# Optimization experiments

Measured on AMD Instinct MI355X. Metric: run time of the kernel, lower is better.

The kernel has to match this reference:

```python
import jax, jax.numpy as jnp
from jax import lax
import numpy as np

UNITS = 256
DYN = 32
STATIC = 27


def setup_inputs() -> dict:
    key = jax.random.key(0)
    ks = jax.random.split(key, 7)
    x_dynamic = jax.random.normal(ks[0], (1024, 365, DYN), dtype=jnp.float32)
    x_static = jax.random.normal(ks[1], (1024, STATIC), dtype=jnp.float32)
    # learned parameters (orthogonal-ish init approximated by scaled normals;
    # weight_hh initialized as tiled identity per the original module)
    weight_ih = jax.random.normal(ks[2], (DYN, 3 * UNITS), dtype=jnp.float32) * 0.1
    eye3 = jnp.concatenate([jnp.eye(UNITS, dtype=jnp.float32)] * 3, axis=1)
    weight_hh = eye3 + jax.random.normal(ks[3], (UNITS, 3 * UNITS), dtype=jnp.float32) * 0.02
    weight_sh = jax.random.normal(ks[4], (STATIC, UNITS), dtype=jnp.float32) * 0.1
    bias = jnp.zeros((3 * UNITS,), dtype=jnp.float32)
    bias_s = jnp.zeros((UNITS,), dtype=jnp.float32)
    return {
        "x_dynamic": x_dynamic,
        "x_static": x_static,
        "weight_ih": weight_ih,
        "weight_hh": weight_hh,
        "weight_sh": weight_sh,
        "bias": bias,
        "bias_s": bias_s,
    }


def reference(x_dynamic, x_static, weight_ih, weight_hh, weight_sh, bias, bias_s):
    B = x_dynamic.shape[0]
    U = weight_sh.shape[1]
    # static input gate, computed once (entity-aware)
    i_gate = jax.nn.sigmoid(x_static @ weight_sh + bias_s)  # [B, U]
    # precompute input contribution for all timesteps: [B, T, 3U]
    gx = jnp.einsum("btd,dk->btk", x_dynamic, weight_ih) + bias
    gx_t = jnp.swapaxes(gx, 0, 1)  # [T, B, 3U] for scan

    h0 = jnp.zeros((B, U), dtype=x_dynamic.dtype)
    c0 = jnp.zeros((B, U), dtype=x_dynamic.dtype)

    def step(carry, g_t):
        h, c = carry
        gates = g_t + h @ weight_hh  # [B, 3U]
        f, o, g = jnp.split(gates, 3, axis=1)
        c_new = jax.nn.sigmoid(f) * c + i_gate * jnp.tanh(g)
        h_new = jax.nn.sigmoid(o) * jnp.tanh(c_new)
        return (h_new, c_new), None

    (h_final, c_final), _ = lax.scan(step, (h0, c0), gx_t)
    return h_final
```

## Files before the change

kernel.cpp:

```cpp
#include <hip/hip_runtime.h>


typedef short short8 __attribute__((ext_vector_type(8)));
typedef short short4s __attribute__((ext_vector_type(4)));
typedef float f32x4 __attribute__((ext_vector_type(4)));
typedef int   i32x4 __attribute__((ext_vector_type(4)));

#define T_STEPS 365
#define UNITS   256
#define G3      768
#define MROWS   4
#define NWGS    256
#define HP8     288
#define XROW    (T_STEPS * 32)
#define XPAD    96
#define WP8_BYTES (256 * G3)

__device__ __forceinline__ unsigned short f2bf(float x) {
    union { float f; unsigned u; } v; v.f = x;
    return (unsigned short)((v.u + 0x7FFFu + ((v.u >> 16) & 1u)) >> 16);
}
__device__ __forceinline__ float rcp_(float x) {
    float r; asm("v_rcp_f32 %0, %1" : "=v"(r) : "v"(x)); return r;
}
__device__ __forceinline__ float sigm_(float x) {
    return rcp_(1.0f + __expf(-x));
}
__device__ __forceinline__ float tanh_(float x) {
    return 1.0f - 2.0f * rcp_(1.0f + __expf(2.0f * x));
}
__device__ __forceinline__ f32x4 MF(short8 a, short8 b, f32x4 c) {
    return __builtin_amdgcn_mfma_f32_16x16x32_bf16(a, b, c, 0, 0, 0);
}
__device__ __forceinline__ i32x4 MI(i32x4 a, i32x4 b, i32x4 c) {
    return __builtin_amdgcn_mfma_i32_16x16x64_i8(a, b, c, 0, 0, 0);
}

__global__ __launch_bounds__(256) void pack_weights(
    const float* __restrict__ w_ih, const float* __restrict__ w_hh,
    signed char* __restrict__ wp8, unsigned short* __restrict__ wpx)
{
    int idx = blockIdx.x * 256 + threadIdx.x;
    if (idx < 256 * G3) {
        const int k = idx / G3, n = idx - k * G3;
        float v = w_hh[k * G3 + n];
        if ((n & 255) == k) v -= 1.0f;
        int q = (int)rintf(v * 1024.0f);
        q = q > 127 ? 127 : (q < -127 ? -127 : q);
        wp8[((size_t)((k >> 6) * G3) + n) * 64 + (k & 63)] = (signed char)q;
    } else if (idx < (256 + 32) * G3) {
        const int idx2 = idx - 256 * G3;
        const int kx = idx2 / G3, n = idx2 - kx * G3;
        wpx[((size_t)((kx >> 3) * G3) + n) * 8 + (kx & 7)] = f2bf(w_ih[kx * G3 + n]);
    }
}

#define STEP_BODY(E, FC, FN, DOX, LOADX, W) do {                              \
    const int p_ = (E) & 1;                                                   \
    __syncthreads();                                                          \
    const signed char* Ap_ = &A_s[p_][0][0];                                  \
    const i32x4 a0_ = *(const i32x4*)(Ap_ + abase);                           \
    const i32x4 a1_ = *(const i32x4*)(Ap_ + abase + 64);                      \
    const i32x4 a2_ = *(const i32x4*)(Ap_ + abase + 128);                     \
    const i32x4 a3_ = *(const i32x4*)(Ap_ + abase + 192);                     \
        \
    i32x4 if0_ = MI(a0_, bwi[0][0][0], IZERO);                                \
    i32x4 io0_ = MI(a0_, bwi[0][1][0], IZERO);                                \
    i32x4 ig0_ = MI(a0_, bwi[0][2][0], IZERO);                                \
    if0_ = MI(a1_, bwi[1][0][0], if0_);                                       \
    io0_ = MI(a1_, bwi[1][1][0], io0_);                                       \
    ig0_ = MI(a1_, bwi[1][2][0], ig0_);                                       \
    if0_ = MI(a2_, bwi[2][0][0], if0_);                                       \
    io0_ = MI(a2_, bwi[2][1][0], io0_);                                       \
    ig0_ = MI(a2_, bwi[2][2][0], ig0_);                                       \
    if0_ = MI(a3_, bwi[3][0][0], if0_);                                       \
    io0_ = MI(a3_, bwi[3][1][0], io0_);                                       \
    ig0_ = MI(a3_, bwi[3][2][0], ig0_);                                       \
    i32x4 if1_ = MI(a0_, bwi[0][0][1], IZERO);                                \
    i32x4 io1_ = MI(a0_, bwi[0][1][1], IZERO);                                \
    i32x4 ig1_ = MI(a0_, bwi[0][2][1], IZERO);                                \
    if1_ = MI(a1_, bwi[1][0][1], if1_);                                       \
    io1_ = MI(a1_, bwi[1][1][1], io1_);                                       \
    ig1_ = MI(a1_, bwi[1][2][1], ig1_);                                       \
    if1_ = MI(a2_, bwi[2][0][1], if1_);                                       \
    io1_ = MI(a2_, bwi[2][1][1], io1_);                                       \
    ig1_ = MI(a2_, bwi[2][2][1], ig1_);                                       \
    if1_ = MI(a3_, bwi[3][0][1], if1_);                                       \
    io1_ = MI(a3_, bwi[3][1][1], io1_);                                       \
    ig1_ = MI(a3_, bwi[3][2][1], ig1_);                                       \
    if (DOX) {                                                                \
           \
        const short8 xu_ = xa;                                                \
        FN[0] = MF(xu_, bwx[0][0], FZERO);                                    \
        FN[1] = MF(xu_, bwx[1][0], FZERO);                                    \
        FN[2] = MF(xu_, bwx[2][0], FZERO);                                    \
        FN[3] = MF(xu_, bwx[0][1], FZERO);                                    \
        FN[4] = MF(xu_, bwx[1][1], FZERO);                                    \
        FN[5] = MF(xu_, bwx[2][1], FZERO);                                    \
        if (LOADX)                                                            \
            xa = *(const short8*)(xq + (size_t)((W) + 2) * 128);              \
    }                                                                         \
    {         \
        const float bh_ = hp[0];                                              \
        const float gf_ = FC[0][E] + bfv[0] + bh_ + (float)if0_[0] * SCL;     \
        const float go_ = FC[1][E] + bov[0] + bh_ + (float)io0_[0] * SCL;     \
        const float gg_ = FC[2][E] + bgv[0] + bh_ + (float)ig0_[0] * SCL;     \
        const float f_  = sigm_(gf_);                                         \
        const float o_  = sigm_(go_);                                         \
        const float gt_ = tanh_(gg_);                                         \
        const float cn_ = f_ * cc[0] + ig[0] * gt_;                           \
        cc[0] = cn_;                                                          \
        const float hn_ = o_ * tanh_(cn_);                                    \
        hp[0] = hn_;                                                          \
        A_s[p_ ^ 1][qq][u0] = (signed char)__float2int_rn(hn_ * 127.0f);      \
    }                                                                         \
    {                                                           \
        const float bh_ = hp[1];                                              \
        const float gf_ = FC[3][E] + bfv[1] + bh_ + (float)if1_[0] * SCL;     \
        const float go_ = FC[4][E] + bov[1] + bh_ + (float)io1_[0] * SCL;     \
        const float gg_ = FC[5][E] + bgv[1] + bh_ + (float)ig1_[0] * SCL;     \
        const float f_  = sigm_(gf_);                                         \
        const float o_  = sigm_(go_);                                         \
        const float gt_ = tanh_(gg_);                                         \
        const float cn_ = f_ * cc[1] + ig[1] * gt_;                           \
        cc[1] = cn_;                                                          \
        const float hn_ = o_ * tanh_(cn_);                                    \
        hp[1] = hn_;                                                          \
        A_s[p_ ^ 1][qq][u1] = (signed char)__float2int_rn(hn_ * 127.0f);      \
    }                                                                         \
} while (0)

#define WINDOW4(W, FC, FN, LOADX) do {                                        \
    STEP_BODY(0, FC, FN, false, false, W);                                    \
    STEP_BODY(1, FC, FN, true,  LOADX, W);                                    \
    STEP_BODY(2, FC, FN, false, false, W);                                    \
    STEP_BODY(3, FC, FN, false, false, W);                                    \
} while (0)

__global__ __launch_bounds__(512, 2) void lstm_mfma(
    const float* __restrict__ x_dyn,
    const float* __restrict__ x_sta,
    const signed char* __restrict__ wp8,
    const unsigned short* __restrict__ wpx,
    const float* __restrict__ w_sh,
    const float* __restrict__ bias,
    const float* __restrict__ bias_s,
    float* __restrict__ out)
{
    __shared__ signed char A_s[2][MROWS][HP8];
    __shared__ unsigned short xs[MROWS * XROW + XPAD];

    const int tid  = threadIdx.x;
    const int b0   = blockIdx.x * MROWS;
    const int lane = tid & 63;
    const int wv   = tid >> 6;
    const int mm   = lane & 15;
    const int qq   = lane >> 4;

    i32x4 bwi[4][3][2];
    #pragma unroll
    for (int ks = 0; ks < 4; ++ks)
        #pragma unroll
        for (int g = 0; g < 3; ++g)
            #pragma unroll
            for (int h = 0; h < 2; ++h) {
                const int n = g * UNITS + wv * 32 + h * 16 + mm;
                bwi[ks][g][h] = *(const i32x4*)(wp8 +
                    ((size_t)(ks * G3) + n) * 64 + qq * 16);
            }
    short8 bwx[3][2];
    #pragma unroll
    for (int g = 0; g < 3; ++g)
        #pragma unroll
        for (int h = 0; h < 2; ++h)
            bwx[g][h] = *(const short8*)(wpx +
                ((size_t)(qq * G3) + g * UNITS + wv * 32 + h * 16 + mm) * 8);

    #pragma unroll
    for (int r = 0; r < MROWS; ++r) {
        const float4* src = (const float4*)(x_dyn + (size_t)(b0 + r) * XROW);
        short4s* dst = (short4s*)(xs + r * XROW);
        for (int i = tid; i < XROW / 4; i += 512) {
            const float4 v = src[i];
            short4s w;
            w.x = (short)f2bf(v.x); w.y = (short)f2bf(v.y);
            w.z = (short)f2bf(v.z); w.w = (short)f2bf(v.w);
            dst[i] = w;
        }
    }
    if (tid < XPAD / 2) ((int*)(xs + MROWS * XROW))[tid] = 0;
    {
        int* az = (int*)A_s;
        for (int i = tid; i < 2 * MROWS * HP8 / 4; i += 512) az[i] = 0;
    }
    __syncthreads();

    const int u0 = wv * 32 + mm;
    const int u1 = u0 + 16;

    const float bfv[2] = { bias[u0],             bias[u1] };
    const float bov[2] = { bias[UNITS + u0],     bias[UNITS + u1] };
    const float bgv[2] = { bias[2 * UNITS + u0], bias[2 * UNITS + u1] };

    float ig[2], cc[2], hp[2];
    #pragma unroll
    for (int h = 0; h < 2; ++h) {
        const int u = h ? u1 : u0;
        float s = bias_s[u];
        #pragma unroll
        for (int j = 0; j < 27; ++j)
            s += x_sta[(b0 + qq) * 27 + j] * w_sh[j * UNITS + u];
        ig[h] = sigm_(s);
        cc[h] = 0.0f; hp[h] = 0.0f;
    }

    const int abase = (mm >> 2) * HP8 + qq * 16;
    const unsigned short* xq = xs + (size_t)(mm >> 2) * XROW + (mm & 3) * 32 + qq * 8;
    const float SCL = 1.0f / (127.0f * 1024.0f);
    const f32x4 FZERO = {0.f, 0.f, 0.f, 0.f};
    const i32x4 IZERO = {0, 0, 0, 0};

    f32x4 FA[6], FB[6];
    short8 xa;
    {
        const short8 x0 = *(const short8*)(xq);
        FA[0] = MF(x0, bwx[0][0], FZERO);
        FA[1] = MF(x0, bwx[1][0], FZERO);
        FA[2] = MF(x0, bwx[2][0], FZERO);
        FA[3] = MF(x0, bwx[0][1], FZERO);
        FA[4] = MF(x0, bwx[1][1], FZERO);
        FA[5] = MF(x0, bwx[2][1], FZERO);
        xa = *(const short8*)(xq + 128);
    }

    for (int wp = 0; wp < 45; ++wp) {
        const int w0 = wp * 2;
        WINDOW4(w0,     FA, FB, true);
        WINDOW4(w0 + 1, FB, FA, true);
    }
    WINDOW4(90, FA, FB, false);
    STEP_BODY(0, FB, FA, false, false, 91);

    out[(size_t)(b0 + qq) * UNITS + u0] = hp[0];
    out[(size_t)(b0 + qq) * UNITS + u1] = hp[1];
}

extern "C" void kernel_launch(void* const* d_in, const int* in_sizes, int n_in,
                              void* d_out, int out_size, void* d_ws, size_t ws_size,
                              hipStream_t stream) {
    const float* x_dyn  = (const float*)d_in[0];
    const float* x_sta  = (const float*)d_in[1];
    const float* w_ih   = (const float*)d_in[2];
    const float* w_hh   = (const float*)d_in[3];
    const float* w_sh   = (const float*)d_in[4];
    const float* bias   = (const float*)d_in[5];
    const float* bias_s = (const float*)d_in[6];
    float* out = (float*)d_out;
    signed char* wp8 = (signed char*)d_ws;
    unsigned short* wpx = (unsigned short*)((char*)d_ws + WP8_BYTES);

    pack_weights<<<((256 + 32) * G3 + 255) / 256, 256, 0, stream>>>(w_ih, w_hh, wp8, wpx);
    lstm_mfma<<<NWGS, 512, 0, stream>>>(x_dyn, x_sta, wp8, wpx, w_sh, bias, bias_s, out);
}
```

Baseline: 348.9 us.

## Split MFMA accumulation chains, raise MFMA priority, pack adjacent-unit h stores

Each gate accumulation is split into two independent MFMA chains (k-slices 0-1 and 2-3) that are summed in integer afterwards, shortening the dependent chain on the recurrent critical path. The MFMA block is wrapped in s_setprio to favour this wave's matrix issue. Each lane now owns units 2*mm and 2*mm+1 instead of mm and mm+16, so the two quantized h bytes go out as one 16-bit LDS store and the final output as a float2 store. This costs extra accumulator registers and integer adds, and changes the weight and bias indexing layout.

```diff
diff --git a/kernel.cpp b/kernel.cpp
--- a/kernel.cpp
+++ b/kernel.cpp
@@ -63,33 +63,22 @@
     const i32x4 a1_ = *(const i32x4*)(Ap_ + abase + 64);                      \
     const i32x4 a2_ = *(const i32x4*)(Ap_ + abase + 128);                     \
     const i32x4 a3_ = *(const i32x4*)(Ap_ + abase + 192);                     \
-        \
-    i32x4 if0_ = MI(a0_, bwi[0][0][0], IZERO);                                \
-    i32x4 io0_ = MI(a0_, bwi[0][1][0], IZERO);                                \
-    i32x4 ig0_ = MI(a0_, bwi[0][2][0], IZERO);                                \
-    if0_ = MI(a1_, bwi[1][0][0], if0_);                                       \
-    io0_ = MI(a1_, bwi[1][1][0], io0_);                                       \
-    ig0_ = MI(a1_, bwi[1][2][0], ig0_);                                       \
-    if0_ = MI(a2_, bwi[2][0][0], if0_);                                       \
-    io0_ = MI(a2_, bwi[2][1][0], io0_);                                       \
-    ig0_ = MI(a2_, bwi[2][2][0], ig0_);                                       \
-    if0_ = MI(a3_, bwi[3][0][0], if0_);                                       \
-    io0_ = MI(a3_, bwi[3][1][0], io0_);                                       \
-    ig0_ = MI(a3_, bwi[3][2][0], ig0_);                                       \
-    i32x4 if1_ = MI(a0_, bwi[0][0][1], IZERO);                                \
-    i32x4 io1_ = MI(a0_, bwi[0][1][1], IZERO);                                \
-    i32x4 ig1_ = MI(a0_, bwi[0][2][1], IZERO);                                \
-    if1_ = MI(a1_, bwi[1][0][1], if1_);                                       \
-    io1_ = MI(a1_, bwi[1][1][1], io1_);                                       \
-    ig1_ = MI(a1_, bwi[1][2][1], ig1_);                                       \
-    if1_ = MI(a2_, bwi[2][0][1], if1_);                                       \
-    io1_ = MI(a2_, bwi[2][1][1], io1_);                                       \
-    ig1_ = MI(a2_, bwi[2][2][1], ig1_);                                       \
-    if1_ = MI(a3_, bwi[3][0][1], if1_);                                       \
-    io1_ = MI(a3_, bwi[3][1][1], io1_);                                       \
-    ig1_ = MI(a3_, bwi[3][2][1], ig1_);                                       \
+    __builtin_amdgcn_s_setprio(1);                                            \
+                     \
+    i32x4 ifA0_ = MI(a1_, bwi[1][0][0], MI(a0_, bwi[0][0][0], IZERO));        \
+    i32x4 ioA0_ = MI(a1_, bwi[1][1][0], MI(a0_, bwi[0][1][0], IZERO));        \
+    i32x4 igA0_ = MI(a1_, bwi[1][2][0], MI(a0_, bwi[0][2][0], IZERO));        \
+    i32x4 ifB0_ = MI(a3_, bwi[3][0][0], MI(a2_, bwi[2][0][0], IZERO));        \
+    i32x4 ioB0_ = MI(a3_, bwi[3][1][0], MI(a2_, bwi[2][1][0], IZERO));        \
+    i32x4 igB0_ = MI(a3_, bwi[3][2][0], MI(a2_, bwi[2][2][0], IZERO));        \
+    i32x4 ifA1_ = MI(a1_, bwi[1][0][1], MI(a0_, bwi[0][0][1], IZERO));        \
+    i32x4 ioA1_ = MI(a1_, bwi[1][1][1], MI(a0_, bwi[0][1][1], IZERO));        \
+    i32x4 igA1_ = MI(a1_, bwi[1][2][1], MI(a0_, bwi[0][2][1], IZERO));        \
+    i32x4 ifB1_ = MI(a3_, bwi[3][0][1], MI(a2_, bwi[2][0][1], IZERO));        \
+    i32x4 ioB1_ = MI(a3_, bwi[3][1][1], MI(a2_, bwi[2][1][1], IZERO));        \
+    i32x4 igB1_ = MI(a3_, bwi[3][2][1], MI(a2_, bwi[2][2][1], IZERO));        \
     if (DOX) {                                                                \
-           \
+                              \
         const short8 xu_ = xa;                                                \
         FN[0] = MF(xu_, bwx[0][0], FZERO);                                    \
         FN[1] = MF(xu_, bwx[1][0], FZERO);                                    \
@@ -100,11 +89,16 @@
         if (LOADX)                                                            \
             xa = *(const short8*)(xq + (size_t)((W) + 2) * 128);              \
     }                                                                         \
-    {         \
+    __builtin_amdgcn_s_setprio(0);                                            \
+    int q0_, q1_;                                                             \
+    {                      \
         const float bh_ = hp[0];                                              \
-        const float gf_ = FC[0][E] + bfv[0] + bh_ + (float)if0_[0] * SCL;     \
-        const float go_ = FC[1][E] + bov[0] + bh_ + (float)io0_[0] * SCL;     \
-        const float gg_ = FC[2][E] + bgv[0] + bh_ + (float)ig0_[0] * SCL;     \
+        const float gf_ = FC[0][E] + bfv[0] + bh_                             \
+                        + (float)(ifA0_[0] + ifB0_[0]) * SCL;                 \
+        const float go_ = FC[1][E] + bov[0] + bh_                             \
+                        + (float)(ioA0_[0] + ioB0_[0]) * SCL;                 \
+        const float gg_ = FC[2][E] + bgv[0] + bh_                             \
+                        + (float)(igA0_[0] + igB0_[0]) * SCL;                 \
         const float f_  = sigm_(gf_);                                         \
         const float o_  = sigm_(go_);                                         \
         const float gt_ = tanh_(gg_);                                         \
@@ -112,13 +106,16 @@
         cc[0] = cn_;                                                          \
         const float hn_ = o_ * tanh_(cn_);                                    \
         hp[0] = hn_;                                                          \
-        A_s[p_ ^ 1][qq][u0] = (signed char)__float2int_rn(hn_ * 127.0f);      \
+        q0_ = __float2int_rn(hn_ * 127.0f);                                   \
     }                                                                         \
     {                                                           \
         const float bh_ = hp[1];                                              \
-        const float gf_ = FC[3][E] + bfv[1] + bh_ + (float)if1_[0] * SCL;     \
-        const float go_ = FC[4][E] + bov[1] + bh_ + (float)io1_[0] * SCL;     \
-        const float gg_ = FC[5][E] + bgv[1] + bh_ + (float)ig1_[0] * SCL;     \
+        const float gf_ = FC[3][E] + bfv[1] + bh_                             \
+                        + (float)(ifA1_[0] + ifB1_[0]) * SCL;                 \
+        const float go_ = FC[4][E] + bov[1] + bh_                             \
+                        + (float)(ioA1_[0] + ioB1_[0]) * SCL;                 \
+        const float gg_ = FC[5][E] + bgv[1] + bh_                             \
+                        + (float)(igA1_[0] + igB1_[0]) * SCL;                 \
         const float f_  = sigm_(gf_);                                         \
         const float o_  = sigm_(go_);                                         \
         const float gt_ = tanh_(gg_);                                         \
@@ -126,8 +123,11 @@
         cc[1] = cn_;                                                          \
         const float hn_ = o_ * tanh_(cn_);                                    \
         hp[1] = hn_;                                                          \
-        A_s[p_ ^ 1][qq][u1] = (signed char)__float2int_rn(hn_ * 127.0f);      \
+        q1_ = __float2int_rn(hn_ * 127.0f);                                   \
     }                                                                         \
+                \
+    *(unsigned short*)&A_s[p_ ^ 1][qq][u0] =                                  \
+        (unsigned short)((q0_ & 0xFF) | ((q1_ & 0xFF) << 8));                 \
 } while (0)
 
 #define WINDOW4(W, FC, FN, LOADX) do {                                        \
@@ -164,7 +164,7 @@
         for (int g = 0; g < 3; ++g)
             #pragma unroll
             for (int h = 0; h < 2; ++h) {
-                const int n = g * UNITS + wv * 32 + h * 16 + mm;
+                const int n = g * UNITS + wv * 32 + 2 * mm + h;
                 bwi[ks][g][h] = *(const i32x4*)(wp8 +
                     ((size_t)(ks * G3) + n) * 64 + qq * 16);
             }
@@ -174,7 +174,7 @@
         #pragma unroll
         for (int h = 0; h < 2; ++h)
             bwx[g][h] = *(const short8*)(wpx +
-                ((size_t)(qq * G3) + g * UNITS + wv * 32 + h * 16 + mm) * 8);
+                ((size_t)(qq * G3) + g * UNITS + wv * 32 + 2 * mm + h) * 8);
 
     #pragma unroll
     for (int r = 0; r < MROWS; ++r) {
@@ -195,17 +195,16 @@
     }
     __syncthreads();
 
-    const int u0 = wv * 32 + mm;
-    const int u1 = u0 + 16;
-
-    const float bfv[2] = { bias[u0],             bias[u1] };
-    const float bov[2] = { bias[UNITS + u0],     bias[UNITS + u1] };
-    const float bgv[2] = { bias[2 * UNITS + u0], bias[2 * UNITS + u1] };
+    const int u0 = wv * 32 + 2 * mm;
+
+    const float bfv[2] = { bias[u0],             bias[u0 + 1] };
+    const float bov[2] = { bias[UNITS + u0],     bias[UNITS + u0 + 1] };
+    const float bgv[2] = { bias[2 * UNITS + u0], bias[2 * UNITS + u0 + 1] };
 
     float ig[2], cc[2], hp[2];
     #pragma unroll
     for (int h = 0; h < 2; ++h) {
-        const int u = h ? u1 : u0;
+        const int u = u0 + h;
         float s = bias_s[u];
         #pragma unroll
         for (int j = 0; j < 27; ++j)
@@ -241,8 +240,10 @@
     WINDOW4(90, FA, FB, false);
     STEP_BODY(0, FB, FA, false, false, 91);
 
-    out[(size_t)(b0 + qq) * UNITS + u0] = hp[0];
-    out[(size_t)(b0 + qq) * UNITS + u1] = hp[1];
+    {
+        float2 o2; o2.x = hp[0]; o2.y = hp[1];
+        *(float2*)(out + (size_t)(b0 + qq) * UNITS + u0) = o2;
+    }
 }
 
 extern "C" void kernel_launch(void* const* d_in, const int* in_sizes, int n_in,
```

New measurement: 356.6 us. 2.2% more time.
